# Optimization experiments

Measured on AMD Instinct MI355X. Metric: run time of the kernel, lower is better.

## Reference

```python
import jax, jax.numpy as jnp
import numpy as np

B, N, F_IN, HID, NHEADS, NCLASS = 256, 200, 768, 32, 8, 2
ALPHA = 0.3          # LeakyReLU negative slope
NEG_INF = -9e15      # mask value used by the torch code for fp32
BN_EPS = 1e-5


def setup_inputs() -> dict:
    key = jax.random.key(0)
    ks = jax.random.split(key, 12)
    xav = lambda k, shape: jax.random.uniform(
        k, shape, jnp.float32, -1.0, 1.0) * 1.414 * np.sqrt(6.0 / (shape[0] + shape[-1]))
    return {
        "feat_matrix": jax.random.normal(ks[0], (B, N, F_IN), jnp.float32),
        "adj": jax.random.randint(ks[1], (B, N, N), 0, 2, jnp.int32),
        # 8 attention heads: W [H, 768, 32], a [H, 64, 1]
        "Wh": xav(ks[2], (NHEADS, F_IN, HID)),
        "ah": xav(ks[3], (NHEADS, 2 * HID, 1)),
        # output GAT layers over concatenated 256-dim features
        "W_sent": xav(ks[4], (HID * NHEADS, NCLASS)),
        "a_sent": xav(ks[5], (2 * NCLASS, 1)),
        "W_para": xav(ks[6], (HID * NHEADS, NCLASS)),
        "a_para": xav(ks[7], (2 * NCLASS, 1)),
        "W_qt": xav(ks[8], (HID * NHEADS, HID)),
        "a_qt": xav(ks[9], (2 * HID, 1)),
        "W2": xav(ks[10], (HID, 2)),
        # BatchNorm1d(nodes_num=200) params/buffers (eval mode)
        "bn_gamma": jnp.ones((N,), jnp.float32),
        "bn_beta": jnp.zeros((N,), jnp.float32),
        "bn_mean": jnp.zeros((N,), jnp.float32),
        "bn_var": jnp.ones((N,), jnp.float32),
    }


def gat_layer(x, mask, W, a, concat):
    # x: [B,N,Fin], W: [Fin,Fout], a: [2*Fout,1]
    h = x @ W                                   # [B,N,Fout]
    fo = W.shape[1]
    s1 = h @ a[:fo, 0]                          # [B,N]  (h_i . a1)
    s2 = h @ a[fo:, 0]                          # [B,N]  (h_j . a2)
    e = jax.nn.leaky_relu(s1[:, :, None] + s2[:, None, :], ALPHA)  # [B,N,N]
    att = jax.nn.softmax(jnp.where(mask, e, NEG_INF), axis=-1)
    out = att @ h                               # [B,N,Fout]
    return jax.nn.elu(out) if concat else out


def reference(feat_matrix, adj, Wh, ah, W_sent, a_sent, W_para, a_para,
              W_qt, a_qt, W2, bn_gamma, bn_beta, bn_mean, bn_var):
    mask = adj > 0                              # [B,N,N]
    # 8 heads, concat -> [B,N,256]
    heads = jax.vmap(lambda W, a: gat_layer(feat_matrix, mask, W, a, True))(Wh, ah)
    x = jnp.transpose(heads, (1, 2, 0, 3)).reshape(B, N, NHEADS * HID)
    # BatchNorm1d over node axis (channels = N), eval mode
    inv = bn_gamma / jnp.sqrt(bn_var + BN_EPS)
    x = (x - bn_mean[None, :, None]) * inv[None, :, None] + bn_beta[None, :, None]
    logits_sent = jax.nn.sigmoid(gat_layer(x, mask, W_sent, a_sent, False))   # [B,N,2]
    logits_para = jax.nn.elu(gat_layer(x, mask, W_para, a_para, False))       # [B,N,2]
    h_qt = gat_layer(x, mask, W_qt, a_qt, False)[:, 0, :]                     # [B,32]
    logits_qtype = jax.nn.elu(h_qt @ W2).reshape(-1, 2)                       # [B,2]
    return logits_sent, logits_para, logits_qtype
```

## Files before the change

### kernel.cpp

```cpp
#include <hip/hip_runtime.h>
#include <hip/hip_bf16.h>

#define ALPHA   0.3f
#define NEG_INF (-9e15f)
#define BN_EPS  1e-5f

typedef _Float16 f16x4 __attribute__((ext_vector_type(4)));
typedef _Float16 f16x8 __attribute__((ext_vector_type(8)));
typedef float    f32x4 __attribute__((ext_vector_type(4)));
typedef unsigned u32x4 __attribute__((ext_vector_type(4)));
typedef unsigned long long u64;

__global__ __launch_bounds__(256) void k_pack(const int* __restrict__ adj,
                                              u64* __restrict__ Mw,
                                              const float* __restrict__ Wh,
                                              _Float16* __restrict__ WT)
{
    if (blockIdx.x < 768) {
        const int o = blockIdx.x * 256 + threadIdx.x;
        const int n = o / 768, k = o - n * 768;
        WT[o] = (_Float16)Wh[((n >> 5) * 768 + k) * 32 + (n & 31)];
    }
    const int w = threadIdx.x >> 6, lane = threadIdx.x & 63;
    const int row = blockIdx.x * 4 + w;
    const int* ar = adj + (size_t)row * 200;
    #pragma unroll
    for (int t = 0; t < 4; ++t) {
        const int j = t * 64 + lane;
        const int a = ar[j < 200 ? j : 199];
        const u64 bal = __ballot(j < 200 && a > 0);
        if (lane == 0) Mw[(size_t)row * 4 + t] = bal;
    }
}

__global__ __launch_bounds__(256) void k_gemm1(const float* __restrict__ A,
                                               const _Float16* __restrict__ WT,
                                               float* __restrict__ H)
{
    __shared__ _Float16 Af[64][72];
    __shared__ _Float16 Bf[256][72];
    const int tid  = threadIdx.x;
    const int wv   = tid >> 6;
    const int lane = tid & 63;
    const int r16  = lane & 15, q = lane >> 4;
    const size_t m_blk = (size_t)blockIdx.x * 64;
    const int wn = wv * 64;
    const int arow = tid >> 2, akb = (tid & 3) * 16;
    f32x4 acc[4][4] = {};

    for (int kt = 0; kt < 768; kt += 64) {
        __syncthreads();
        #pragma unroll
        for (int p = 0; p < 4; ++p) {
            const float4 a4 = *(const float4*)&A[(m_blk + arow) * 768 + kt + akb + p * 4];
            f16x4 h4 = { (_Float16)a4.x, (_Float16)a4.y, (_Float16)a4.z, (_Float16)a4.w };
            *(f16x4*)&Af[arow][akb + p * 4] = h4;
        }
        #pragma unroll
        for (int p = 0; p < 8; ++p) {
            f16x8 w8 = *(const f16x8*)&WT[tid * 768 + kt + p * 8];
            *(f16x8*)&Bf[tid][p * 8] = w8;
        }
        __syncthreads();
        #pragma unroll
        for (int kc = 0; kc < 64; kc += 32) {
            f16x8 af[4], bf[4];
            #pragma unroll
            for (int i = 0; i < 4; ++i)
                af[i] = *(const f16x8*)&Af[i * 16 + r16][kc + q * 8];
            #pragma unroll
            for (int j = 0; j < 4; ++j)
                bf[j] = *(const f16x8*)&Bf[wn + j * 16 + r16][kc + q * 8];
            #pragma unroll
            for (int i = 0; i < 4; ++i)
                #pragma unroll
                for (int j = 0; j < 4; ++j)
                    acc[i][j] = __builtin_amdgcn_mfma_f32_16x16x32_f16(
                        af[i], bf[j], acc[i][j], 0, 0, 0);
        }
    }
    #pragma unroll
    for (int i = 0; i < 4; ++i)
        #pragma unroll
        for (int j = 0; j < 4; ++j)
            #pragma unroll
            for (int r = 0; r < 4; ++r) {
                const int m = i * 16 + q * 4 + r;
                const int n = wn + j * 16 + r16;
                H[(m_blk + m) * 256 + n] = acc[i][j][r];
            }
}

__global__ __launch_bounds__(512, 4) void k_attn1(float* __restrict__ H,
    const unsigned* __restrict__ Mw, const float* __restrict__ ah,
    const float* __restrict__ bng, const float* __restrict__ bnb,
    const float* __restrict__ bnm, const float* __restrict__ bnv)
{
    __shared__ alignas(16) _Float16 HsT[32][232];
    __shared__ alignas(16) unsigned Ml[208][8];
    __shared__ alignas(16) float s2[224];
    __shared__ alignas(16) float s1[208];
    __shared__ float bnA[208], bnB[208];
    const int tid  = threadIdx.x;
    const int b    = blockIdx.x >> 3;
    const int head = blockIdx.x & 7;
    float* Hb = H + (size_t)b * 200 * 256 + head * 32;
    const unsigned* Mb = Mw + (size_t)b * 200 * 8;

    if (tid < 256) {
        for (int idx = tid; idx < 6400; idx += 256) {
            int n = idx >> 5, f = idx & 31;
            HsT[f][n] = (_Float16)Hb[n * 256 + f];
        }
        for (int idx = tid; idx < 32 * 32; idx += 256) {
            int f = idx >> 5, c = 200 + (idx & 31);
            HsT[f][c] = (_Float16)0.f;
        }
    } else if (tid < 456) {
        const int row = tid - 256;
        const float* avg = ah + head * 64;
        float v1 = 0.f, v2 = 0.f;
        #pragma unroll
        for (int f = 0; f < 32; f += 4) {
            const float4 h4 = *(const float4*)&Hb[row * 256 + f];
            const float4 a1 = *(const float4*)&avg[f];
            const float4 a2 = *(const float4*)&avg[32 + f];
            v1 += h4.x * a1.x + h4.y * a1.y + h4.z * a1.z + h4.w * a1.w;
            v2 += h4.x * a2.x + h4.y * a2.y + h4.z * a2.z + h4.w * a2.w;
        }
        s1[row] = v1; s2[row] = v2;
        const float iv = bng[row] * rsqrtf(bnv[row] + BN_EPS);
        bnA[row] = iv; bnB[row] = bnb[row] - bnm[row] * iv;
    } else {
        const int t2 = tid - 456;
        for (int idx = t2; idx < 416; idx += 56) {
            const int rr = idx >> 1, hf = idx & 1;
            u32x4 mv = {0u, 0u, 0u, 0u};
            if (rr < 200) mv = *(const u32x4*)&Mb[rr * 8 + hf * 4];
            *(u32x4*)&Ml[rr][hf * 4] = mv;
        }
        if (t2 < 8)  s1[200 + t2] = 0.f;
        if (t2 >= 8 && t2 < 32) s2[200 + (t2 - 8)] = 0.f;
    }
    __syncthreads();

    const int lane = tid & 63, wv = tid >> 6;
    const int r16 = lane & 15, q = lane >> 4;

    for (int tile = wv; tile < 13; tile += 8) {
        const int m0  = tile * 16;
        const int row = m0 + r16;
        const float s1i = s1[row];
        const u32x4 mwa = *(const u32x4*)&Ml[row][0];
        const u32x4 mwb = *(const u32x4*)&Ml[row][4];
        const unsigned mw[7] = {mwa[0], mwa[1], mwa[2], mwa[3],
                                mwb[0], mwb[1], mwb[2]};

        float m = -INFINITY;
        #pragma unroll
        for (int ks = 0; ks < 7; ++ks) {
            const f32x4 sA = *(const f32x4*)&s2[ks * 32 + q * 8];
            const f32x4 sB = *(const f32x4*)&s2[ks * 32 + q * 8 + 4];
            const unsigned wb = mw[ks] >> (q * 8);
            #pragma unroll
            for (int e = 0; e < 8; ++e) {
                const float sv = (e < 4) ? sA[e] : sB[e - 4];
                const float t = s1i + sv;
                const float tl = fmaxf(t, ALPHA * t);
                m = fmaxf(m, ((wb >> e) & 1u) ? tl : -INFINITY);
            }
        }
        m = fmaxf(m, __shfl_xor(m, 16));
        m = fmaxf(m, __shfl_xor(m, 32));

        float s = 0.f;
        f16x8 pa[7];
        #pragma unroll
        for (int ks = 0; ks < 7; ++ks) {
            const f32x4 sA = *(const f32x4*)&s2[ks * 32 + q * 8];
            const f32x4 sB = *(const f32x4*)&s2[ks * 32 + q * 8 + 4];
            const unsigned wb = mw[ks] >> (q * 8);
            #pragma unroll
            for (int e = 0; e < 8; ++e) {
                const float sv = (e < 4) ? sA[e] : sB[e - 4];
                float t = s1i + sv;
                t = fmaxf(t, ALPHA * t);
                float pe = __expf(t - m);
                pe = ((wb >> e) & 1u) ? pe : 0.f;
                s += pe;
                pa[ks][e] = (_Float16)pe;
            }
        }
        s += __shfl_xor(s, 16);
        s += __shfl_xor(s, 32);
        const float sinv = 1.f / s;

        f32x4 acc0 = {0.f, 0.f, 0.f, 0.f}, acc1 = {0.f, 0.f, 0.f, 0.f};
        #pragma unroll
        for (int ks = 0; ks < 7; ++ks) {
            const int k0 = ks * 32 + q * 8;
            const f16x8 b0 = *(const f16x8*)&HsT[r16][k0];
            const f16x8 b1 = *(const f16x8*)&HsT[16 + r16][k0];
            acc0 = __builtin_amdgcn_mfma_f32_16x16x32_f16(pa[ks], b0, acc0, 0, 0, 0);
            acc1 = __builtin_amdgcn_mfma_f32_16x16x32_f16(pa[ks], b1, acc1, 0, 0, 0);
        }
        float rv[4];
        #pragma unroll
        for (int r = 0; r < 4; ++r) rv[r] = __shfl(sinv, q * 4 + r);
        #pragma unroll
        for (int r = 0; r < 4; ++r) {
            const int i = m0 + q * 4 + r;
            if (i < 200) {
                float o0 = acc0[r] * rv[r];
                float o1 = acc1[r] * rv[r];
                o0 = o0 > 0.f ? o0 : expm1f(o0);
                o1 = o1 > 0.f ? o1 : expm1f(o1);
                const float ga = bnA[i], gb = bnB[i];
                Hb[i * 256 + r16]      = o0 * ga + gb;
                Hb[i * 256 + 16 + r16] = o1 * ga + gb;
            }
        }
    }
}

__global__ __launch_bounds__(256) void k_gemm2(const float* __restrict__ X,
    const float* __restrict__ Ws, const float* __restrict__ Wp,
    const float* __restrict__ Wq, float* __restrict__ Y)
{
    __shared__ float Wl[256][48];
    __shared__ float XsT[64][68];
    const int tid = threadIdx.x;
    {
        const int k = tid;
        #pragma unroll
        for (int c = 0; c < 36; ++c) {
            float v;
            if      (c == 0) v = Ws[k * 2 + 0];
            else if (c == 1) v = Ws[k * 2 + 1];
            else if (c == 2) v = Wp[k * 2 + 0];
            else if (c == 3) v = Wp[k * 2 + 1];
            else             v = Wq[k * 32 + (c - 4)];
            Wl[k][12 * (c / 9) + (c % 9)] = v;
        }
    }
    const int r  = tid & 63;
    const int cg = tid >> 6;
    const size_t row0 = (size_t)blockIdx.x * 64;
    float acc[9] = {};

    for (int kt = 0; kt < 256; kt += 64) {
        __syncthreads();
        #pragma unroll
        for (int i = 0; i < 4; ++i) {
            int l = tid + 256 * i;
            int row = l >> 4;
            int k4 = (l & 15) * 4;
            const float4 x4 = *(const float4*)&X[(row0 + row) * 256 + kt + k4];
            XsT[k4 + 0][row] = x4.x; XsT[k4 + 1][row] = x4.y;
            XsT[k4 + 2][row] = x4.z; XsT[k4 + 3][row] = x4.w;
        }
        __syncthreads();
        #pragma unroll 4
        for (int k = 0; k < 64; ++k) {
            const float xv = XsT[k][r];
            const float4 w0 = *(const float4*)&Wl[kt + k][12 * cg + 0];
            const float4 w1 = *(const float4*)&Wl[kt + k][12 * cg + 4];
            const float  w2 = Wl[kt + k][12 * cg + 8];
            acc[0] += xv * w0.x; acc[1] += xv * w0.y;
            acc[2] += xv * w0.z; acc[3] += xv * w0.w;
            acc[4] += xv * w1.x; acc[5] += xv * w1.y;
            acc[6] += xv * w1.z; acc[7] += xv * w1.w;
            acc[8] += xv * w2;
        }
    }
    float* yr = Y + (row0 + r) * 36 + cg * 9;
    #pragma unroll
    for (int c = 0; c < 9; ++c) yr[c] = acc[c];
}

__global__ __launch_bounds__(512, 4) void k_attn2(const float* __restrict__ Y,
    const int* __restrict__ adj, const float* __restrict__ a_s,
    const float* __restrict__ a_p, const float* __restrict__ a_q,
    const float* __restrict__ W2, float* __restrict__ out)
{
    __shared__ float Ys[200][37];
    __shared__ float s1s[200], s2s[200], p1s[200], p2s[200], sq2[200];
    __shared__ float p0[200];
    __shared__ float hqt[32];
    __shared__ float sumq_s;
    __shared__ float asl[4], apl[4], aql[64], w2l[64];
    const int tid  = threadIdx.x;
    const int b    = blockIdx.x >> 1;
    const int half = blockIdx.x & 1;
    const float* Yb = Y + (size_t)b * 7200;
    const int* adjb = adj + (size_t)b * 200 * 200;

    for (int idx = tid; idx < 7200; idx += 512) {
        int j = idx / 36;
        int c = idx - j * 36;
        Ys[j][c] = Yb[idx];
    }
    if (tid < 4)  { asl[tid] = a_s[tid]; apl[tid] = a_p[tid]; }
    if (tid >= 64 && tid < 128) { aql[tid - 64] = a_q[tid - 64]; w2l[tid - 64] = W2[tid - 64]; }
    __syncthreads();

    if (tid < 200) {
        int j = tid;
        s1s[j] = Ys[j][0] * asl[0] + Ys[j][1] * asl[1];
        s2s[j] = Ys[j][0] * asl[2] + Ys[j][1] * asl[3];
        p1s[j] = Ys[j][2] * apl[0] + Ys[j][3] * apl[1];
        p2s[j] = Ys[j][2] * apl[2] + Ys[j][3] * apl[3];
        float a = 0.f;
        #pragma unroll
        for (int f = 0; f < 32; ++f) a += Ys[j][4 + f] * aql[32 + f];
        sq2[j] = a;
    }
    __syncthreads();

    const int w = tid >> 6, lane = tid & 63;
    for (int ii = w; ii < 100; ii += 8) {
        const int i = half * 100 + ii;
        const float s1i = s1s[i], p1i = p1s[i];
        float ms = -INFINITY, mp = -INFINITY;
        float es[4], ep[4];
        #pragma unroll
        for (int t = 0; t < 4; ++t) {
            int j = lane + 64 * t;
            int jj = j < 200 ? j : 0;
            int a = (j < 200) ? adjb[i * 200 + j] : 0;
            float e1 = s1i + s2s[jj]; e1 = e1 >= 0.f ? e1 : ALPHA * e1;
            float e2 = p1i + p2s[jj]; e2 = e2 >= 0.f ? e2 : ALPHA * e2;
            es[t] = (a > 0) ? e1 : (j < 200 ? NEG_INF : -INFINITY);
            ep[t] = (a > 0) ? e2 : (j < 200 ? NEG_INF : -INFINITY);
            ms = fmaxf(ms, es[t]); mp = fmaxf(mp, ep[t]);
        }
        #pragma unroll
        for (int off = 32; off >= 1; off >>= 1) {
            ms = fmaxf(ms, __shfl_xor(ms, off));
            mp = fmaxf(mp, __shfl_xor(mp, off));
        }
        float ss = 0.f, sp = 0.f, os0 = 0.f, os1 = 0.f, op0 = 0.f, op1 = 0.f;
        #pragma unroll
        for (int t = 0; t < 4; ++t) {
            int j = lane + 64 * t;
            int jj = j < 200 ? j : 0;
            float pes = __expf(es[t] - ms);
            float pep = __expf(ep[t] - mp);
            ss += pes; sp += pep;
            os0 += pes * Ys[jj][0]; os1 += pes * Ys[jj][1];
            op0 += pep * Ys[jj][2]; op1 += pep * Ys[jj][3];
        }
        #pragma unroll
        for (int off = 32; off >= 1; off >>= 1) {
            ss  += __shfl_xor(ss, off);  sp  += __shfl_xor(sp, off);
            os0 += __shfl_xor(os0, off); os1 += __shfl_xor(os1, off);
            op0 += __shfl_xor(op0, off); op1 += __shfl_xor(op1, off);
        }
        if (lane == 0) {
            float v0 = os0 / ss, v1 = os1 / ss;
            out[((size_t)b * 200 + i) * 2 + 0] = 1.f / (1.f + __expf(-v0));
            out[((size_t)b * 200 + i) * 2 + 1] = 1.f / (1.f + __expf(-v1));
            float q0 = op0 / sp, q1 = op1 / sp;
            out[102400 + ((size_t)b * 200 + i) * 2 + 0] = q0 > 0.f ? q0 : expm1f(q0);
            out[102400 + ((size_t)b * 200 + i) * 2 + 1] = q1 > 0.f ? q1 : expm1f(q1);
        }
    }

    if (half == 0 && tid < 64) {
        float s1q = 0.f;
        #pragma unroll
        for (int f = 0; f < 32; ++f) s1q += Ys[0][4 + f] * aql[f];
        float mq = -INFINITY;
        float eq[4];
        #pragma unroll
        for (int t = 0; t < 4; ++t) {
            int j = tid + 64 * t;
            int jj = j < 200 ? j : 0;
            int a = (j < 200) ? adjb[j] : 0;
            float e = s1q + sq2[jj]; e = e >= 0.f ? e : ALPHA * e;
            eq[t] = (a > 0) ? e : (j < 200 ? NEG_INF : -INFINITY);
            mq = fmaxf(mq, eq[t]);
        }
        #pragma unroll
        for (int off = 32; off >= 1; off >>= 1) mq = fmaxf(mq, __shfl_xor(mq, off));
        float sq = 0.f;
        #pragma unroll
        for (int t = 0; t < 4; ++t) {
            int j = tid + 64 * t;
            float pe = __expf(eq[t] - mq);
            sq += pe;
            if (j < 200) p0[j] = pe;
        }
        #pragma unroll
        for (int off = 32; off >= 1; off >>= 1) sq += __shfl_xor(sq, off);
        if (tid == 0) sumq_s = sq;
    }
    __syncthreads();
    if (half == 0 && tid < 32) {
        float acc = 0.f;
        for (int j = 0; j < 200; ++j) acc += p0[j] * Ys[j][4 + tid];
        hqt[tid] = acc / sumq_s;
    }
    __syncthreads();
    if (half == 0 && tid < 2) {
        float v = 0.f;
        #pragma unroll
        for (int f = 0; f < 32; ++f) v += hqt[f] * w2l[f * 2 + tid];
        out[204800 + (size_t)b * 2 + tid] = v > 0.f ? v : expm1f(v);
    }
}

extern "C" void kernel_launch(void* const* d_in, const int* in_sizes, int n_in,
                              void* d_out, int out_size, void* d_ws, size_t ws_size,
                              hipStream_t stream) {
    const float* feat   = (const float*)d_in[0];
    const int*   adj    = (const int*)  d_in[1];
    const float* Wh     = (const float*)d_in[2];
    const float* ah     = (const float*)d_in[3];
    const float* W_sent = (const float*)d_in[4];
    const float* a_sent = (const float*)d_in[5];
    const float* W_para = (const float*)d_in[6];
    const float* a_para = (const float*)d_in[7];
    const float* W_qt   = (const float*)d_in[8];
    const float* a_qt   = (const float*)d_in[9];
    const float* W2     = (const float*)d_in[10];
    const float* bng    = (const float*)d_in[11];
    const float* bnb    = (const float*)d_in[12];
    const float* bnm    = (const float*)d_in[13];
    const float* bnv    = (const float*)d_in[14];

    float* H = (float*)d_ws;
    float* Y = H + (size_t)51200 * 256;
    _Float16* WT = (_Float16*)(Y + (size_t)51200 * 36);
    u64* Mw = (u64*)Y;
    float* out = (float*)d_out;

    k_pack<<<12800, 256, 0, stream>>>(adj, Mw, Wh, WT);
    k_gemm1<<<800, 256, 0, stream>>>(feat, WT, H);
    k_attn1<<<2048, 512, 0, stream>>>(H, (const unsigned*)Mw, ah, bng, bnb, bnm, bnv);
    k_gemm2<<<800, 256, 0, stream>>>(H, W_sent, W_para, W_qt, Y);
    k_attn2<<<512, 512, 0, stream>>>(Y, adj, a_sent, a_para, a_qt, W2, out);
}
```

Before: 566.8 us.

## Shrink attn1 blocks to 256 threads, coalesce H loads, reorder grid head-major

Cuts the first attention kernel's block size from 512 to 256 threads and raises the occupancy hint from 4 to 6 blocks per CU. Each wave now handles up to 4 row tiles instead of 1-2. The H staging now uses float4 loads: 8 lanes cooperate per node, each writes the transposed fp16 tile and computes a partial s1/s2 dot product reduced with shuffles, replacing the separate scalar row-dot pass. The grid is reordered so consecutive blocks share a head across batches, which changes L2 locality. The aim is less idle-thread waste during staging and higher occupancy, at the cost of more serial tile work per wave.

After: 609.4 us. 7.5% more time.

```diff
diff --git a/kernel.cpp b/kernel.cpp
--- a/kernel.cpp
+++ b/kernel.cpp
@@ -91,7 +91,7 @@
             }
 }
 
-__global__ __launch_bounds__(512, 4) void k_attn1(float* __restrict__ H,
+__global__ __launch_bounds__(256, 6) void k_attn1(float* __restrict__ H,
     const unsigned* __restrict__ Mw, const float* __restrict__ ah,
     const float* __restrict__ bng, const float* __restrict__ bnb,
     const float* __restrict__ bnm, const float* __restrict__ bnv)
@@ -102,52 +102,54 @@
     __shared__ alignas(16) float s1[208];
     __shared__ float bnA[208], bnB[208];
     const int tid  = threadIdx.x;
-    const int b    = blockIdx.x >> 3;
-    const int head = blockIdx.x & 7;
+    const int b    = blockIdx.x & 255;
+    const int head = blockIdx.x >> 8;
     float* Hb = H + (size_t)b * 200 * 256 + head * 32;
     const unsigned* Mb = Mw + (size_t)b * 200 * 8;
 
-    if (tid < 256) {
-        for (int idx = tid; idx < 6400; idx += 256) {
-            int n = idx >> 5, f = idx & 31;
-            HsT[f][n] = (_Float16)Hb[n * 256 + f];
-        }
-        for (int idx = tid; idx < 32 * 32; idx += 256) {
-            int f = idx >> 5, c = 200 + (idx & 31);
-            HsT[f][c] = (_Float16)0.f;
-        }
-    } else if (tid < 456) {
-        const int row = tid - 256;
-        const float* avg = ah + head * 64;
-        float v1 = 0.f, v2 = 0.f;
-        #pragma unroll
-        for (int f = 0; f < 32; f += 4) {
-            const float4 h4 = *(const float4*)&Hb[row * 256 + f];
-            const float4 a1 = *(const float4*)&avg[f];
-            const float4 a2 = *(const float4*)&avg[32 + f];
-            v1 += h4.x * a1.x + h4.y * a1.y + h4.z * a1.z + h4.w * a1.w;
-            v2 += h4.x * a2.x + h4.y * a2.y + h4.z * a2.z + h4.w * a2.w;
-        }
-        s1[row] = v1; s2[row] = v2;
-        const float iv = bng[row] * rsqrtf(bnv[row] + BN_EPS);
-        bnA[row] = iv; bnB[row] = bnb[row] - bnm[row] * iv;
-    } else {
-        const int t2 = tid - 456;
-        for (int idx = t2; idx < 416; idx += 56) {
-            const int rr = idx >> 1, hf = idx & 1;
-            u32x4 mv = {0u, 0u, 0u, 0u};
-            if (rr < 200) mv = *(const u32x4*)&Mb[rr * 8 + hf * 4];
-            *(u32x4*)&Ml[rr][hf * 4] = mv;
-        }
-        if (t2 < 8)  s1[200 + t2] = 0.f;
-        if (t2 >= 8 && t2 < 32) s2[200 + (t2 - 8)] = 0.f;
+    const int fq = tid & 7;
+    const int gn = tid >> 3;
+    const float4 a1 = *(const float4*)&ah[head * 64 + fq * 4];
+    const float4 a2 = *(const float4*)&ah[head * 64 + 32 + fq * 4];
+    #pragma unroll
+    for (int it = 0; it < 7; ++it) {
+        const int n = gn + 32 * it;
+        if (n < 200) {
+            const float4 h4 = *(const float4*)&Hb[n * 256 + fq * 4];
+            HsT[fq * 4 + 0][n] = (_Float16)h4.x;
+            HsT[fq * 4 + 1][n] = (_Float16)h4.y;
+            HsT[fq * 4 + 2][n] = (_Float16)h4.z;
+            HsT[fq * 4 + 3][n] = (_Float16)h4.w;
+            float v1 = h4.x * a1.x + h4.y * a1.y + h4.z * a1.z + h4.w * a1.w;
+            float v2 = h4.x * a2.x + h4.y * a2.y + h4.z * a2.z + h4.w * a2.w;
+            v1 += __shfl_xor(v1, 1); v2 += __shfl_xor(v2, 1);
+            v1 += __shfl_xor(v1, 2); v2 += __shfl_xor(v2, 2);
+            v1 += __shfl_xor(v1, 4); v2 += __shfl_xor(v2, 4);
+            if (fq == 0) { s1[n] = v1; s2[n] = v2; }
+        }
+    }
+    for (int idx = tid; idx < 32 * 32; idx += 256) {
+        int f = idx >> 5, c = 200 + (idx & 31);
+        HsT[f][c] = (_Float16)0.f;
+    }
+    for (int idx = tid; idx < 416; idx += 256) {
+        const int rr = idx >> 1, hf = idx & 1;
+        u32x4 mv = {0u, 0u, 0u, 0u};
+        if (rr < 200) mv = *(const u32x4*)&Mb[rr * 8 + hf * 4];
+        *(u32x4*)&Ml[rr][hf * 4] = mv;
+    }
+    if (tid < 8) s1[200 + tid] = 0.f;
+    if (tid >= 8 && tid < 32) s2[200 + (tid - 8)] = 0.f;
+    if (tid < 200) {
+        const float iv = bng[tid] * rsqrtf(bnv[tid] + BN_EPS);
+        bnA[tid] = iv; bnB[tid] = bnb[tid] - bnm[tid] * iv;
     }
     __syncthreads();
 
     const int lane = tid & 63, wv = tid >> 6;
     const int r16 = lane & 15, q = lane >> 4;
 
-    for (int tile = wv; tile < 13; tile += 8) {
+    for (int tile = wv; tile < 13; tile += 4) {
         const int m0  = tile * 16;
         const int row = m0 + r16;
         const float s1i = s1[row];
@@ -437,7 +439,7 @@
 
     k_pack<<<12800, 256, 0, stream>>>(adj, Mw, Wh, WT);
     k_gemm1<<<800, 256, 0, stream>>>(feat, WT, H);
-    k_attn1<<<2048, 512, 0, stream>>>(H, (const unsigned*)Mw, ah, bng, bnb, bnm, bnv);
+    k_attn1<<<2048, 256, 0, stream>>>(H, (const unsigned*)Mw, ah, bng, bnb, bnm, bnv);
     k_gemm2<<<800, 256, 0, stream>>>(H, W_sent, W_para, W_qt, Y);
     k_attn2<<<512, 512, 0, stream>>>(Y, adj, a_sent, a_para, a_qt, W2, out);
 }
```
